# Kernel tuning notes

Hardware: AMD Instinct MI355X
Metric: run time of the kernel (lower is better)

The kernel has to match this reference:

```python
import jax, jax.numpy as jnp
import numpy as np

B, C_IN, C_OUT, H, W, K, NK = 16, 256, 256, 64, 64, 3, 2
EPS = 1e-8


def setup_inputs() -> dict:
    key = jax.random.key(0)
    k1, k2, k3, k4 = jax.random.split(key, 4)
    x = jax.random.normal(k1, (B, C_IN, H, W), dtype=jnp.float32)
    mod = jax.random.normal(k2, (B, C_IN), dtype=jnp.float32)
    kernel_mod = jax.random.normal(k3, (B, NK), dtype=jnp.float32)
    # kernel bank: [num_conv_kernels, dim_out, dim_in, k, k] (kaiming-ish scale)
    weights = jax.random.normal(k4, (NK, C_OUT, C_IN, K, K), dtype=jnp.float32) / np.sqrt(C_IN * K * K)
    gamma = jnp.ones((C_OUT,), dtype=jnp.float32)
    return {"x": x, "mod": mod, "kernel_mod": kernel_mod, "weights": weights, "gamma": gamma}


def _block(x, mod, kernel_mod, weights, gamma):
    # adaptive kernel selection: softmax-mix the kernel bank per sample
    attn = jax.nn.softmax(kernel_mod, axis=-1)                       # [b, n]
    w = jnp.einsum('bn,noikl->boikl', attn, weights)                 # [b, o, i, k, k]
    # style modulation over input channels
    w = w * (mod[:, None, :, None, None] + 1.0)
    # demodulation
    denom = jnp.clip(jnp.sum(w * w, axis=(2, 3, 4), keepdims=True), EPS)
    w = w * jax.lax.rsqrt(denom)
    # per-sample conv (groups=b trick in torch) -> vmap over batch
    def conv_one(fmap, wb):
        return jax.lax.conv_general_dilated(
            fmap[None], wb, window_strides=(1, 1), padding='SAME',
            dimension_numbers=('NCHW', 'OIHW', 'NCHW'))[0]
    y = jax.vmap(conv_one)(x, w)                                     # [b, o, h, w]
    # RMSNorm over channel dim: F.normalize(x, dim=1) * gamma * sqrt(dim)
    norm = jnp.sqrt(jnp.sum(y * y, axis=1, keepdims=True))
    y = y / jnp.maximum(norm, 1e-12)
    y = y * gamma[None, :, None, None] * (gamma.shape[0] ** 0.5)
    # SiLU
    return y * jax.nn.sigmoid(y)


def reference(x, mod, kernel_mod, weights, gamma):
    return _block(x, mod, kernel_mod, weights, gamma)
```

## Files before the change

### kernel.cpp

```cpp
#include <hip/hip_runtime.h>
#include <math.h>


typedef __attribute__((ext_vector_type(8))) short short8;
typedef __attribute__((ext_vector_type(16))) float f32x16;

#define GLL16(src, dst)                                                       \
  __builtin_amdgcn_global_load_lds(                                           \
      (const __attribute__((address_space(1))) unsigned int*)(src),           \
      (__attribute__((address_space(3))) unsigned int*)(dst), 16, 0, 0)

static __device__ __forceinline__ unsigned short f2bf(float v) {
  union { float f; unsigned u; } u;
  u.f = v;
  unsigned r = u.u + 0x7FFF + ((u.u >> 16) & 1);
  return (unsigned short)(r >> 16);
}

__global__ __launch_bounds__(256) void wprep(
    const float* __restrict__ mod, const float* __restrict__ kmod,
    const float* __restrict__ weights, unsigned short* __restrict__ wq) {
  int blk = blockIdx.x;
  int b = blk >> 5, oq = blk & 31;
  int t = threadIdx.x;
  int o_l = t >> 5, its = t & 31;
  int o = oq * 8 + o_l;

  float k0 = kmod[b * 2 + 0], k1 = kmod[b * 2 + 1];
  float mx = fmaxf(k0, k1);
  float e0 = expf(k0 - mx), e1 = expf(k1 - mx);
  float ai = 1.0f / (e0 + e1);
  float a0 = e0 * ai, a1 = e1 * ai;

  float wv[9][8];
  float s = 0.0f;
  const float* w0 = &weights[((size_t)o * 256 + its * 8) * 9];
  const float* w1 = w0 + 589824;
#pragma unroll
  for (int e = 0; e < 8; ++e) {
    float f = mod[b * 256 + its * 8 + e] + 1.0f;
#pragma unroll
    for (int j = 0; j < 9; ++j) {
      float v = (a0 * w0[e * 9 + j] + a1 * w1[e * 9 + j]) * f;
      wv[j][e] = v;
      s = fmaf(v, v, s);
    }
  }

  __shared__ float red[8][32];
  __shared__ float scl[8];
  red[o_l][its] = s;
  __syncthreads();
  if (t < 8) {
    float tot = 0.0f;
#pragma unroll
    for (int k = 0; k < 32; ++k) tot += red[t][k];
    scl[t] = rsqrtf(fmaxf(tot, 1e-8f));
  }
  __syncthreads();
  float sc = scl[o_l];

  int c = its >> 1, io = its & 1;
  int oh = o >> 7, mf = (o >> 5) & 3;
  int lane2 = (o & 31) + io * 32;
  size_t cbase = ((size_t)(b * 16 + c)) * 36864 + oh * 2048 + mf * 512 + lane2 * 8;
#pragma unroll
  for (int j = 0; j < 9; ++j) {
    short8 pk;
#pragma unroll
    for (int e = 0; e < 8; ++e) pk[e] = (short)f2bf(wv[j][e] * sc);
    *(short8*)(wq + cbase + j * 4096) = pk;
  }
}

__global__ __launch_bounds__(256) void xprep(
    const float* __restrict__ x, unsigned short* __restrict__ xq) {
  int blk = blockIdx.x;
  int rowp = blk % 66;
  int bc = blk / 66;
  int b = bc >> 4, c = bc & 15;
  int t = threadIdx.x;
  size_t obase = (size_t)blk * 1056;

  if (rowp == 0 || rowp == 65) {
    for (int idx = t; idx < 1056; idx += 256) xq[obase + idx] = 0;
    return;
  }
  __shared__ __align__(16) unsigned short xs2[1056];
  int row = rowp - 1;
  for (int idx = t; idx < 1056; idx += 256) xs2[idx] = 0;
  __syncthreads();
#pragma unroll
  for (int k = 0; k < 4; ++k) {
    int idx = t + k * 256;
    int il = idx >> 6, col = idx & 63;
    float v = x[(((size_t)b * 256 + c * 16 + il) * 64 + row) * 64 + col];
    xs2[(col + 1) * 16 + il] = f2bf(v);
  }
  __syncthreads();
  if (t < 132) *(short8*)(xq + obase + (size_t)t * 8) = *(const short8*)&xs2[t * 8];
}

__global__ __launch_bounds__(512, 2) void conv_fused(
    const unsigned short* __restrict__ xq, const unsigned short* __restrict__ wq,
    const float* __restrict__ gamma, float* __restrict__ out) {
  __shared__ __align__(16) unsigned short wsm[36864];
  __shared__ __align__(16) unsigned short xsm[2][8192];
  __shared__ float redl[1024];
  __shared__ float invs[256];
  __shared__ float gsm[256];

  int bid = blockIdx.x;
  int xcd = bid & 7;
  int kk = bid >> 3;
  int b = xcd * 2 + (kk >> 4);
  int rt = kk & 15;
  int r0 = rt * 4;

  int t = threadIdx.x;
  int w = t >> 6, lane = t & 63;
  int oh = w & 1, ps = w >> 1;
  int l31 = lane & 31, l5 = lane >> 5;

  if (t < 256) gsm[t] = gamma[t];

  const char* aw = (const char*)wsm + oh * 4096 + lane * 16;
  const char* xb0 = (const char*)xsm[0] + (ps * 66 + l31) * 32 + l5 * 16;
  const char* xb1 = (const char*)xsm[1] + (ps * 66 + l31) * 32 + l5 * 16;

  f32x16 acc[4][2];
#pragma unroll
  for (int mf = 0; mf < 4; ++mf)
#pragma unroll
    for (int h = 0; h < 2; ++h)
#pragma unroll
      for (int q = 0; q < 16; ++q) acc[mf][h][q] = 0.f;

#define GLLL(cn)                                                               \
  _Pragma("unroll") for (int r = 0; r < 4; ++r) {                              \
    GLL16(wq + ((size_t)(b * 16 + (cn))) * 36864 + (r * 512 + t) * 8,          \
          &wsm[(r * 512 + t) * 8]);                                            \
  }
#define GLLH(cn)                                                               \
  _Pragma("unroll") for (int r = 0; r < 5; ++r) {                              \
    GLL16(wq + ((size_t)(b * 16 + (cn))) * 36864 + 16384 + (r * 512 + t) * 8,  \
          &wsm[16384 + (r * 512 + t) * 8]);                                    \
  }
#define GLLX(cn, nb)                                                           \
  _Pragma("unroll") for (int r = 0; r < 2; ++r) {                              \
    GLL16(xq + ((size_t)((b * 16 + (cn)) * 66 + r0)) * 1056 + (r * 512 + t) * 8, \
          &xsm[nb][(r * 512 + t) * 8]);                                        \
  }

#define TAP(T, xbp)                                                            \
  {                                                                            \
    short8 A[4], Bv[2];                                                        \
    _Pragma("unroll") for (int mf = 0; mf < 4; ++mf)                           \
        A[mf] = *(const short8*)(aw + (T) * 8192 + mf * 1024);                 \
    _Pragma("unroll") for (int h = 0; h < 2; ++h)                              \
        Bv[h] = *(const short8*)((xbp) + ((T) / 3) * 2112 + ((T) % 3) * 32 +   \
                                 h * 1024);                                    \
    _Pragma("unroll") for (int h = 0; h < 2; ++h)                              \
        _Pragma("unroll") for (int mf = 0; mf < 4; ++mf)                       \
            acc[mf][h] = __builtin_amdgcn_mfma_f32_32x32x16_bf16(              \
                A[mf], Bv[h], acc[mf][h], 0, 0, 0);                            \
  }

#define SBAR __builtin_amdgcn_sched_barrier(0)
#define LGKM0 asm volatile("s_waitcnt lgkmcnt(0)" ::: "memory")
#define VM0 asm volatile("s_waitcnt vmcnt(0)" ::: "memory")
#define BAR __builtin_amdgcn_s_barrier()

  GLLL(0); GLLH(0); GLLX(0, 0);
  VM0;
  BAR;
  SBAR;

  for (int c = 0; c < 16; ++c) {
    const char* xbp = (c & 1) ? xb1 : xb0;
    TAP(0, xbp); TAP(1, xbp); TAP(2, xbp); TAP(3, xbp);
    LGKM0;
    VM0;
    SBAR;
    BAR;
    SBAR;
    if (c < 15) { GLLL(c + 1); GLLX(c + 1, (c & 1) ^ 1); }
    TAP(4, xbp); TAP(5, xbp); TAP(6, xbp); TAP(7, xbp); TAP(8, xbp);
    LGKM0;
    VM0;
    SBAR;
    BAR;
    SBAR;
    if (c < 15) { GLLH(c + 1); }
  }

#pragma unroll
  for (int h = 0; h < 2; ++h) {
    float pssum = 0.f;
#pragma unroll
    for (int mf = 0; mf < 4; ++mf)
#pragma unroll
      for (int q = 0; q < 16; ++q) {
        float v = acc[mf][h][q];
        pssum = fmaf(v, v, pssum);
      }
    int px = ps * 64 + h * 32 + l31;
    redl[(oh * 2 + l5) * 256 + px] = pssum;
  }
  __syncthreads();
  if (t < 256) {
    float ssum = redl[t] + redl[256 + t] + redl[512 + t] + redl[768 + t];
    invs[t] = 16.0f / fmaxf(sqrtf(ssum), 1e-12f);
  }
  __syncthreads();
  float iv2[2];
#pragma unroll
  for (int h = 0; h < 2; ++h) iv2[h] = invs[ps * 64 + h * 32 + l31];

#pragma unroll
  for (int mf = 0; mf < 4; ++mf)
#pragma unroll
    for (int q = 0; q < 16; ++q) {
      int o = oh * 128 + mf * 32 + (q & 3) + 8 * (q >> 2) + 4 * l5;
      float g = gsm[o];
      size_t ob = ((size_t)b * 256 + o) * 64 + (r0 + ps);
#pragma unroll
      for (int h = 0; h < 2; ++h) {
        float v = acc[mf][h][q] * iv2[h] * g;
        float sg = 1.0f / (1.0f + expf(-v));
        out[ob * 64 + h * 32 + l31] = v * sg;
      }
    }
#undef GLLL
#undef GLLH
#undef GLLX
#undef TAP
#undef SBAR
#undef LGKM0
#undef VM0
#undef BAR
}

extern "C" void kernel_launch(void* const* d_in, const int* in_sizes, int n_in,
                              void* d_out, int out_size, void* d_ws, size_t ws_size,
                              hipStream_t stream) {
  const float* x = (const float*)d_in[0];
  const float* mod = (const float*)d_in[1];
  const float* kmod = (const float*)d_in[2];
  const float* weights = (const float*)d_in[3];
  const float* gamma = (const float*)d_in[4];
  float* out = (float*)d_out;

  unsigned short* xq = (unsigned short*)d_ws;
  unsigned short* wq = (unsigned short*)((char*)d_ws + 35684352);

  wprep<<<512, 256, 0, stream>>>(mod, kmod, weights, wq);
  xprep<<<16 * 16 * 66, 256, 0, stream>>>(x, xq);
  conv_fused<<<256, 512, 0, stream>>>(xq, wq, gamma, out);
}
```

Baseline: 121.0 us.

## Software-pipeline LDS fragment reads with MFMA and swizzle x layout against bank conflicts

Double-buffers the A/B register fragments so the LDS reads for the next tap are issued before the MFMAs of the current tap, including prefetching tap 0 of the next channel across the loop barrier. It also XOR-swizzles the 16-byte halves of each column in the packed x layout, with matching offsets in the conv reads, to reduce LDS bank conflicts. MFMA blocks are wrapped in s_setprio to favour matrix issue. The cost is higher register pressure from the extra fragment buffers and precomputed offsets under the 2-wave occupancy bound.

```diff
diff --git a/kernel.cpp b/kernel.cpp
--- a/kernel.cpp
+++ b/kernel.cpp
@@ -98,7 +98,11 @@
     xs2[(col + 1) * 16 + il] = f2bf(v);
   }
   __syncthreads();
-  if (t < 132) *(short8*)(xq + obase + (size_t)t * 8) = *(const short8*)&xs2[t * 8];
+  if (t < 132) {
+    int colp = t >> 1, io = t & 1;
+    int d = colp * 2 + (io ^ (colp & 1));
+    *(short8*)(xq + obase + (size_t)d * 8) = *(const short8*)&xs2[t * 8];
+  }
 }
 
 __global__ __launch_bounds__(512, 2) void conv_fused(
@@ -125,8 +129,13 @@
   if (t < 256) gsm[t] = gamma[t];
 
   const char* aw = (const char*)wsm + oh * 4096 + lane * 16;
-  const char* xb0 = (const char*)xsm[0] + (ps * 66 + l31) * 32 + l5 * 16;
-  const char* xb1 = (const char*)xsm[1] + (ps * 66 + l31) * 32 + l5 * 16;
+  int boffs[9];
+#pragma unroll
+  for (int T = 0; T < 9; ++T) {
+    int kh = T / 3, kw = T % 3;
+    int base = (ps + kh) * 2112 + (l31 + kw) * 32 + l5 * 16;
+    boffs[T] = base ^ ((((l31 + kw) & 1)) << 4);
+  }
 
   f32x16 acc[4][2];
 #pragma unroll
@@ -152,18 +161,24 @@
           &xsm[nb][(r * 512 + t) * 8]);                                        \
   }
 
-#define TAP(T, xbp)                                                            \
+  short8 PA[4], PB[2], QA[4], QB[2];
+
+#define DSRD(SA, SB, T, xsb_)                                                  \
   {                                                                            \
-    short8 A[4], Bv[2];                                                        \
     _Pragma("unroll") for (int mf = 0; mf < 4; ++mf)                           \
-        A[mf] = *(const short8*)(aw + (T) * 8192 + mf * 1024);                 \
+        SA[mf] = *(const short8*)(aw + (T) * 8192 + mf * 1024);                \
     _Pragma("unroll") for (int h = 0; h < 2; ++h)                              \
-        Bv[h] = *(const short8*)((xbp) + ((T) / 3) * 2112 + ((T) % 3) * 32 +   \
-                                 h * 1024);                                    \
+        SB[h] = *(const short8*)((xsb_) + boffs[T] + h * 1024);                \
+  }
+
+#define MFMA8(SA, SB)                                                          \
+  {                                                                            \
+    __builtin_amdgcn_s_setprio(1);                                             \
     _Pragma("unroll") for (int h = 0; h < 2; ++h)                              \
         _Pragma("unroll") for (int mf = 0; mf < 4; ++mf)                       \
             acc[mf][h] = __builtin_amdgcn_mfma_f32_32x32x16_bf16(              \
-                A[mf], Bv[h], acc[mf][h], 0, 0, 0);                            \
+                SA[mf], SB[h], acc[mf][h], 0, 0, 0);                           \
+    __builtin_amdgcn_s_setprio(0);                                             \
   }
 
 #define SBAR __builtin_amdgcn_sched_barrier(0)
@@ -171,27 +186,45 @@
 #define VM0 asm volatile("s_waitcnt vmcnt(0)" ::: "memory")
 #define BAR __builtin_amdgcn_s_barrier()
 
+  const char* xs0 = (const char*)xsm[0];
+  const char* xs1 = (const char*)xsm[1];
+
   GLLL(0); GLLH(0); GLLX(0, 0);
   VM0;
   BAR;
   SBAR;
+  DSRD(PA, PB, 0, xs0);
+  SBAR;
 
   for (int c = 0; c < 16; ++c) {
-    const char* xbp = (c & 1) ? xb1 : xb0;
-    TAP(0, xbp); TAP(1, xbp); TAP(2, xbp); TAP(3, xbp);
+    const char* xsb = (c & 1) ? xs1 : xs0;
+    const char* xsn = (c & 1) ? xs0 : xs1;
+    DSRD(QA, QB, 1, xsb); SBAR; MFMA8(PA, PB);
+    DSRD(PA, PB, 2, xsb); SBAR; MFMA8(QA, QB);
+    DSRD(QA, QB, 3, xsb); SBAR; MFMA8(PA, PB);
+    SBAR; MFMA8(QA, QB);
     LGKM0;
     VM0;
     SBAR;
     BAR;
     SBAR;
     if (c < 15) { GLLL(c + 1); GLLX(c + 1, (c & 1) ^ 1); }
-    TAP(4, xbp); TAP(5, xbp); TAP(6, xbp); TAP(7, xbp); TAP(8, xbp);
+    DSRD(PA, PB, 4, xsb); SBAR;
+    DSRD(QA, QB, 5, xsb); SBAR; MFMA8(PA, PB);
+    DSRD(PA, PB, 6, xsb); SBAR; MFMA8(QA, QB);
+    DSRD(QA, QB, 7, xsb); SBAR; MFMA8(PA, PB);
+    DSRD(PA, PB, 8, xsb); SBAR; MFMA8(QA, QB);
+    SBAR; MFMA8(PA, PB);
     LGKM0;
     VM0;
     SBAR;
     BAR;
     SBAR;
-    if (c < 15) { GLLH(c + 1); }
+    if (c < 15) {
+      GLLH(c + 1);
+      DSRD(PA, PB, 0, xsn);
+      SBAR;
+    }
   }
 
 #pragma unroll
@@ -234,7 +267,8 @@
 #undef GLLL
 #undef GLLH
 #undef GLLX
-#undef TAP
+#undef DSRD
+#undef MFMA8
 #undef SBAR
 #undef LGKM0
 #undef VM0
```

Measured after the change: 120.4 us. No clear change (-0.5%).

## Stream conv weights from global into double-buffered registers instead of LDS

Applied to the files above, without the earlier changes.

Weight fragments are no longer staged through LDS. Each wave now loads its A fragments directly from global memory into two alternating register sets, one tap ahead, interleaved with the LDS reads of the input tile and the MFMAs. MFMA issue priority is raised with s_setprio, and the loop drops from two block barriers per channel chunk to one, with a partial vmcnt wait. This frees about 72KB of LDS and removes weight staging stalls. In exchange, the four pixel-strip waves that share the same weights now each fetch them separately through the cache hierarchy, and the loop depends on global load latency being hidden one tap ahead.

```diff
diff --git a/kernel.cpp b/kernel.cpp
--- a/kernel.cpp
+++ b/kernel.cpp
@@ -104,7 +104,6 @@
 __global__ __launch_bounds__(512, 2) void conv_fused(
     const unsigned short* __restrict__ xq, const unsigned short* __restrict__ wq,
     const float* __restrict__ gamma, float* __restrict__ out) {
-  __shared__ __align__(16) unsigned short wsm[36864];
   __shared__ __align__(16) unsigned short xsm[2][8192];
   __shared__ float redl[1024];
   __shared__ float invs[256];
@@ -124,9 +123,12 @@
 
   if (t < 256) gsm[t] = gamma[t];
 
-  const char* aw = (const char*)wsm + oh * 4096 + lane * 16;
-  const char* xb0 = (const char*)xsm[0] + (ps * 66 + l31) * 32 + l5 * 16;
-  const char* xb1 = (const char*)xsm[1] + (ps * 66 + l31) * 32 + l5 * 16;
+  int boffs[9];
+#pragma unroll
+  for (int T = 0; T < 9; ++T) {
+    int kh = T / 3, kw = T % 3;
+    boffs[T] = (ps + kh) * 2112 + (l31 + kw) * 32 + l5 * 16;
+  }
 
   f32x16 acc[4][2];
 #pragma unroll
@@ -136,62 +138,74 @@
 #pragma unroll
       for (int q = 0; q < 16; ++q) acc[mf][h][q] = 0.f;
 
-#define GLLL(cn)                                                               \
-  _Pragma("unroll") for (int r = 0; r < 4; ++r) {                              \
-    GLL16(wq + ((size_t)(b * 16 + (cn))) * 36864 + (r * 512 + t) * 8,          \
-          &wsm[(r * 512 + t) * 8]);                                            \
-  }
-#define GLLH(cn)                                                               \
-  _Pragma("unroll") for (int r = 0; r < 5; ++r) {                              \
-    GLL16(wq + ((size_t)(b * 16 + (cn))) * 36864 + 16384 + (r * 512 + t) * 8,  \
-          &wsm[16384 + (r * 512 + t) * 8]);                                    \
-  }
 #define GLLX(cn, nb)                                                           \
   _Pragma("unroll") for (int r = 0; r < 2; ++r) {                              \
     GLL16(xq + ((size_t)((b * 16 + (cn)) * 66 + r0)) * 1056 + (r * 512 + t) * 8, \
           &xsm[nb][(r * 512 + t) * 8]);                                        \
   }
 
-#define TAP(T, xbp)                                                            \
-  {                                                                            \
-    short8 A[4], Bv[2];                                                        \
+#define AGLB(SA, CC, TT)                                                       \
+  {                                                                            \
+    const unsigned short* ap_ = wq + (size_t)(b * 16 + (CC)) * 36864 +         \
+                                (TT) * 4096 + oh * 2048 + lane * 8;            \
     _Pragma("unroll") for (int mf = 0; mf < 4; ++mf)                           \
-        A[mf] = *(const short8*)(aw + (T) * 8192 + mf * 1024);                 \
+        SA[mf] = *(const short8*)(ap_ + mf * 512);                             \
+  }
+
+#define BDSRD(SB, T, XB)                                                       \
+  {                                                                            \
     _Pragma("unroll") for (int h = 0; h < 2; ++h)                              \
-        Bv[h] = *(const short8*)((xbp) + ((T) / 3) * 2112 + ((T) % 3) * 32 +   \
-                                 h * 1024);                                    \
+        SB[h] = *(const short8*)((XB) + boffs[T] + h * 1024);                  \
+  }
+
+#define MFMA8(SA, SB)                                                          \
+  {                                                                            \
+    __builtin_amdgcn_s_setprio(1);                                             \
     _Pragma("unroll") for (int h = 0; h < 2; ++h)                              \
         _Pragma("unroll") for (int mf = 0; mf < 4; ++mf)                       \
             acc[mf][h] = __builtin_amdgcn_mfma_f32_32x32x16_bf16(              \
-                A[mf], Bv[h], acc[mf][h], 0, 0, 0);                            \
+                SA[mf], SB[h], acc[mf][h], 0, 0, 0);                           \
+    __builtin_amdgcn_s_setprio(0);                                             \
   }
 
 #define SBAR __builtin_amdgcn_sched_barrier(0)
-#define LGKM0 asm volatile("s_waitcnt lgkmcnt(0)" ::: "memory")
-#define VM0 asm volatile("s_waitcnt vmcnt(0)" ::: "memory")
 #define BAR __builtin_amdgcn_s_barrier()
 
-  GLLL(0); GLLH(0); GLLX(0, 0);
-  VM0;
+  short8 PA[4], QA[4], PB[2], QB[2];
+
+  const char* xs0 = (const char*)xsm[0];
+  const char* xs1 = (const char*)xsm[1];
+
+#define STEP(C, A0, A1, XB)                                                    \
+  {                                                                            \
+    int CN = (C) < 15 ? (C) + 1 : 15;                                          \
+    GLLX(CN, ((C)&1) ^ 1);                                                     \
+    BDSRD(PB, 0, XB); SBAR;                                                    \
+    BDSRD(QB, 1, XB); SBAR; MFMA8(A0, PB); AGLB(A0, (C), 2); SBAR;             \
+    BDSRD(PB, 2, XB); SBAR; MFMA8(A1, QB); AGLB(A1, (C), 3); SBAR;             \
+    BDSRD(QB, 3, XB); SBAR; MFMA8(A0, PB); AGLB(A0, (C), 4); SBAR;             \
+    BDSRD(PB, 4, XB); SBAR; MFMA8(A1, QB); AGLB(A1, (C), 5); SBAR;             \
+    BDSRD(QB, 5, XB); SBAR; MFMA8(A0, PB); AGLB(A0, (C), 6); SBAR;             \
+    BDSRD(PB, 6, XB); SBAR; MFMA8(A1, QB); AGLB(A1, (C), 7); SBAR;             \
+    BDSRD(QB, 7, XB); SBAR; MFMA8(A0, PB); AGLB(A0, (C), 8); SBAR;             \
+    BDSRD(PB, 8, XB); SBAR; MFMA8(A1, QB); AGLB(A1, CN, 0); SBAR;              \
+    MFMA8(A0, PB); AGLB(A0, CN, 1); SBAR;                                      \
+    asm volatile("s_waitcnt vmcnt(8) lgkmcnt(0)" ::: "memory");                \
+    BAR;                                                                       \
+    SBAR;                                                                      \
+  }
+
+  GLLX(0, 0);
+  asm volatile("s_waitcnt vmcnt(0)" ::: "memory");
   BAR;
   SBAR;
-
-  for (int c = 0; c < 16; ++c) {
-    const char* xbp = (c & 1) ? xb1 : xb0;
-    TAP(0, xbp); TAP(1, xbp); TAP(2, xbp); TAP(3, xbp);
-    LGKM0;
-    VM0;
-    SBAR;
-    BAR;
-    SBAR;
-    if (c < 15) { GLLL(c + 1); GLLX(c + 1, (c & 1) ^ 1); }
-    TAP(4, xbp); TAP(5, xbp); TAP(6, xbp); TAP(7, xbp); TAP(8, xbp);
-    LGKM0;
-    VM0;
-    SBAR;
-    BAR;
-    SBAR;
-    if (c < 15) { GLLH(c + 1); }
+  AGLB(PA, 0, 0);
+  AGLB(QA, 0, 1);
+  SBAR;
+
+  for (int cc = 0; cc < 16; cc += 2) {
+    STEP(cc, PA, QA, xs0);
+    STEP(cc + 1, QA, PA, xs1);
   }
 
 #pragma unroll
@@ -231,14 +245,13 @@
         out[ob * 64 + h * 32 + l31] = v * sg;
       }
     }
-#undef GLLL
-#undef GLLH
 #undef GLLX
-#undef TAP
+#undef AGLB
+#undef BDSRD
+#undef MFMA8
 #undef SBAR
-#undef LGKM0
-#undef VM0
 #undef BAR
+#undef STEP
 }
 
 extern "C" void kernel_launch(void* const* d_in, const int* in_sizes, int n_in,
```

Result: slower. 124.5 us (+2.8%).
